# Performance work log

Measured on AMD Instinct MI355X. Metric: run time of the kernel, lower is better.

The kernel has to match this reference:

```python
import jax, jax.numpy as jnp
import numpy as np


def setup_inputs() -> dict:
    key = jax.random.key(0)
    kZ, kQ, kW, kU, kbk = jax.random.split(key, 5)
    B, E, D = 64, 16, 64
    N_ATOMS = 200000
    N_NP = 160000
    N_BK = 20000
    Q_DIM = 64
    Z = jax.random.normal(kZ, (B, E, D), dtype=jnp.float32)
    Q = jax.random.normal(kQ, (B, Q_DIM), dtype=jnp.float32)
    W = jax.random.normal(kW, (N_NP, D), dtype=jnp.float32)
    U = jax.random.normal(kU, (N_NP, Q_DIM), dtype=jnp.float32)
    np_indices = jnp.arange(N_NP, dtype=jnp.int64 if jax.config.jax_enable_x64 else jnp.int32)
    bk_indices = jax.random.randint(kbk, (N_BK,), 0, N_ATOMS, dtype=jnp.int32)
    return {"Z": Z, "Q": Q, "W": W, "U": U,
            "np_indices": np_indices, "bk_indices": bk_indices,
            "n_atoms": N_ATOMS}


def reference(Z, Q, W, U, np_indices, bk_indices, n_atoms):
    # Batched valuation for all neural-predicate atoms at once:
    # vm(Z, Q, atom_i) = sigmoid(sum_{e,d} Z[b,e,d] * W[i,d] + Q[b] . U[i])
    scores = jax.nn.sigmoid(jnp.einsum('bed,nd->bn', Z, W) + Q @ U.T)  # [B, n_np]
    B = Z.shape[0]
    V = jnp.zeros((B, n_atoms), dtype=jnp.float32)
    V = V.at[:, 0].set(1.0)                 # V[:, 0] = 1.0 (true atom)
    V = V.at[:, np_indices].set(scores)     # scatter valuation outputs
    V = V.at[:, bk_indices].add(1.0)        # background knowledge atoms += 1
    return V
```

## Files before the change

kernel.cpp:

```cpp
#include <hip/hip_runtime.h>


typedef _Float16 half8_t __attribute__((ext_vector_type(8)));
typedef float float4_t __attribute__((ext_vector_type(4)));

#define E_DIM 16
#define D_DIM 64
#define QD    64
#define NS    2
#define CRES_STRIDE 132

__global__ void prep_kernel(const float* __restrict__ Z, const float* __restrict__ Q,
                            const int* __restrict__ bk, int n_bk,
                            _Float16* __restrict__ Afrag, float* __restrict__ cnt) {
    int blk = blockIdx.x;
    int tid = threadIdx.x;
    if (blk < 32) {
        int t = blk * 256 + tid;
        int b = t >> 7, k = t & 127;
        float v;
        if (k < D_DIM) {
            const float* zp = Z + (size_t)b * E_DIM * D_DIM + k;
            v = 0.f;
            #pragma unroll
            for (int e = 0; e < E_DIM; ++e) v += zp[e * D_DIM];
        } else {
            v = Q[b * QD + (k - D_DIM)];
        }
        int mt = b >> 4, r = b & 15;
        int kq = k >> 5, j = k & 7, quad = (k >> 3) & 3;
        int lane = r + quad * 16;
        Afrag[(((mt * 4 + kq) * 64) + lane) * 8 + j] = (_Float16)v;
    } else if (cnt) {
        int i = (blk - 32) * 256 + tid;
        if (i < n_bk) atomicAdd(&cnt[bk[i]], 1.0f);
    }
}

__global__ __launch_bounds__(256, 3) void main_kernel(
        const float* __restrict__ W, const float* __restrict__ U,
        const _Float16* __restrict__ Afrag, const float* __restrict__ cnt,
        float* __restrict__ V, int n_np, int n_atoms, int tail_w) {
    __shared__ __align__(16) half8_t Ash[1024];
    __shared__ __align__(16) float Cres[64][CRES_STRIDE];
    int tid = threadIdx.x;
    int bid = blockIdx.x;
    long long base = (long long)bid * (64 * NS);
    int wv = tid >> 6, lane = tid & 63;
    int quad = lane >> 4, l15 = lane & 15;
    int rB = wv * 16 + l15;

    const float4_t* Wg = (const float4_t*)W;
    const float4_t* Ug = (const float4_t*)U;

    {
        const half8_t* Ap = (const half8_t*)Afrag;
        #pragma unroll
        for (int i = 0; i < 4; ++i)
            Ash[tid + i * 256] = Ap[tid + i * 256];
    }

    int cfl = tid & 31;
    float4_t cn4 = {0.f, 0.f, 0.f, 0.f};
    if (cnt) cn4 = *(const float4_t*)(cnt + base + 4 * cfl);

    {
        long long tb = (long long)n_np + (long long)bid * tail_w;
        int c8 = tid & 7, rg = tid >> 3;
        long long col = tb + 4 * c8;
        if (4 * c8 < tail_w && col < n_atoms) {
            float4_t t4 = {0.f, 0.f, 0.f, 0.f};
            if (cnt) t4 = *(const float4_t*)(cnt + col);
            *(float4_t*)(V + (size_t)rg * n_atoms + col) = t4;
            *(float4_t*)(V + (size_t)(rg + 32) * n_atoms + col) = t4;
        }
    }

    __syncthreads();

    auto load_panel = [&](int s, float4_t wr[4], float4_t ur[4]) {
        size_t o = ((size_t)(base + s * 64 + rB)) * 16 + quad * 2;
        wr[0] = Wg[o];     wr[1] = Wg[o + 1];
        wr[2] = Wg[o + 8]; wr[3] = Wg[o + 9];
        ur[0] = Ug[o];     ur[1] = Ug[o + 1];
        ur[2] = Ug[o + 8]; ur[3] = Ug[o + 9];
    };

    auto compute_panel = [&](int s, const float4_t wr[4], const float4_t ur[4]) {
        half8_t b0, b1, b2, b3;
        #pragma unroll
        for (int q = 0; q < 4; ++q) {
            b0[q]     = (_Float16)wr[0][q];
            b0[q + 4] = (_Float16)wr[1][q];
            b1[q]     = (_Float16)wr[2][q];
            b1[q + 4] = (_Float16)wr[3][q];
            b2[q]     = (_Float16)ur[0][q];
            b2[q + 4] = (_Float16)ur[1][q];
            b3[q]     = (_Float16)ur[2][q];
            b3[q + 4] = (_Float16)ur[3][q];
        }
        #pragma unroll
        for (int mt = 0; mt < 4; ++mt) {
            half8_t a0 = Ash[(mt * 4 + 0) * 64 + lane];
            half8_t a1 = Ash[(mt * 4 + 1) * 64 + lane];
            half8_t a2 = Ash[(mt * 4 + 2) * 64 + lane];
            half8_t a3 = Ash[(mt * 4 + 3) * 64 + lane];
            float4_t acc = {0.f, 0.f, 0.f, 0.f};
            acc = __builtin_amdgcn_mfma_f32_16x16x32_f16(a0, b0, acc, 0, 0, 0);
            acc = __builtin_amdgcn_mfma_f32_16x16x32_f16(a1, b1, acc, 0, 0, 0);
            acc = __builtin_amdgcn_mfma_f32_16x16x32_f16(a2, b2, acc, 0, 0, 0);
            acc = __builtin_amdgcn_mfma_f32_16x16x32_f16(a3, b3, acc, 0, 0, 0);
            #pragma unroll
            for (int r = 0; r < 4; ++r)
                Cres[mt * 16 + quad * 4 + r][s * 64 + rB] = acc[r];
        }
    };

    float4_t w0[4], u0[4], w1[4], u1[4];
    load_panel(0, w0, u0);
    {
    }
    compute_panel(0, w0, u0);
    load_panel(1, w1, u1);
    compute_panel(1, w1, u1);

    __syncthreads();

    #pragma unroll
    for (int rd = 0; rd < 8; ++rd) {
        int row = rd * 8 + (tid >> 5);
        float4_t v = *(const float4_t*)&Cres[row][4 * cfl];
        float4_t out;
        #pragma unroll
        for (int q = 0; q < 4; ++q)
            out[q] = 1.0f / (1.0f + __expf(-v[q])) + cn4[q];
        *(float4_t*)(V + (size_t)row * n_atoms + base + 4 * cfl) = out;
    }
}

__global__ void bk_scatter(const int* __restrict__ bk, int n_bk,
                           float* __restrict__ V, int n_atoms) {
    int i = blockIdx.x * 256 + threadIdx.x;
    if (i < n_bk)
        atomicAdd(&V[(size_t)blockIdx.y * n_atoms + bk[i]], 1.0f);
}

extern "C" void kernel_launch(void* const* d_in, const int* in_sizes, int n_in,
                              void* d_out, int out_size, void* d_ws, size_t ws_size,
                              hipStream_t stream) {
    const float* Z = (const float*)d_in[0];
    const float* Q = (const float*)d_in[1];
    const float* W = (const float*)d_in[2];
    const float* U = (const float*)d_in[3];
    const int* bk = (const int*)d_in[5];
    float* V = (float*)d_out;

    int B       = in_sizes[0] / (E_DIM * D_DIM);
    int n_np    = in_sizes[2] / D_DIM;
    int n_bk    = in_sizes[5];
    int n_atoms = out_size / B;

    _Float16* Afrag = (_Float16*)d_ws;
    size_t need = 16384 + (size_t)n_atoms * sizeof(float);
    bool use_cnt = ws_size >= need;
    float* cnt = use_cnt ? (float*)((char*)d_ws + 16384) : nullptr;

    if (use_cnt) {
        hipMemsetAsync(cnt, 0, (size_t)n_atoms * sizeof(float), stream);
        int cnt_blocks = (n_bk + 255) / 256;
        prep_kernel<<<32 + cnt_blocks, 256, 0, stream>>>(Z, Q, bk, n_bk, Afrag, cnt);
    } else {
        prep_kernel<<<32, 256, 0, stream>>>(Z, Q, bk, n_bk, Afrag, nullptr);
    }

    int gb = n_np / (64 * NS);
    int tail_w = (n_atoms - n_np + gb - 1) / gb;
    main_kernel<<<gb, 256, 0, stream>>>(W, U, Afrag, cnt, V,
                                        n_np, n_atoms, tail_w);

    if (!use_cnt) {
        dim3 g((n_bk + 255) / 256, B);
        bk_scatter<<<g, 256, 0, stream>>>(bk, n_bk, V, n_atoms);
    }
}
```

Measured before the change: 139.7 us.

## Process five panels per block with double-buffered loads and per-panel epilogue

Each block now handles five 64-column panels instead of two, and prefetches W/U two panels ahead into a two-slot register buffer. The sigmoid epilogue runs per panel through a smaller 64x68 LDS tile guarded by custom lgkmcnt barriers, so V stores overlap the next panel's loads. Tail-region zeroing becomes a strided loop, and occupancy is lowered to 2 blocks per SM. The aim is fewer blocks, less setup per block and better overlap of loads with MFMA work, at the cost of extra barriers. The tail width is now floor-divided, which only covers every column when the remainder divides evenly, as it does for these sizes.

```diff
diff --git a/kernel.cpp b/kernel.cpp
--- a/kernel.cpp
+++ b/kernel.cpp
@@ -7,8 +7,16 @@
 #define E_DIM 16
 #define D_DIM 64
 #define QD    64
-#define NS    2
-#define CRES_STRIDE 132
+#define NP    5
+#define CRES_STRIDE 68
+
+__device__ __forceinline__ void lds_barrier() {
+    asm volatile("s_waitcnt lgkmcnt(0)" ::: "memory");
+    __builtin_amdgcn_sched_barrier(0);
+    __builtin_amdgcn_s_barrier();
+    __builtin_amdgcn_sched_barrier(0);
+    asm volatile("" ::: "memory");
+}
 
 __global__ void prep_kernel(const float* __restrict__ Z, const float* __restrict__ Q,
                             const int* __restrict__ bk, int n_bk,
@@ -37,7 +45,7 @@
     }
 }
 
-__global__ __launch_bounds__(256, 3) void main_kernel(
+__global__ __launch_bounds__(256, 2) void main_kernel(
         const float* __restrict__ W, const float* __restrict__ U,
         const _Float16* __restrict__ Afrag, const float* __restrict__ cnt,
         float* __restrict__ V, int n_np, int n_atoms, int tail_w) {
@@ -45,10 +53,12 @@
     __shared__ __align__(16) float Cres[64][CRES_STRIDE];
     int tid = threadIdx.x;
     int bid = blockIdx.x;
-    long long base = (long long)bid * (64 * NS);
+    long long base = (long long)bid * (64 * NP);
     int wv = tid >> 6, lane = tid & 63;
     int quad = lane >> 4, l15 = lane & 15;
     int rB = wv * 16 + l15;
+    int chunk = tid & 15;
+    int rgrp  = tid >> 4;
 
     const float4_t* Wg = (const float4_t*)W;
     const float4_t* Ug = (const float4_t*)U;
@@ -60,45 +70,63 @@
             Ash[tid + i * 256] = Ap[tid + i * 256];
     }
 
-    int cfl = tid & 31;
-    float4_t cn4 = {0.f, 0.f, 0.f, 0.f};
-    if (cnt) cn4 = *(const float4_t*)(cnt + base + 4 * cfl);
+    float4_t cn4[NP];
+    #pragma unroll
+    for (int p = 0; p < NP; ++p) {
+        cn4[p] = float4_t{0.f, 0.f, 0.f, 0.f};
+        if (cnt) cn4[p] = *(const float4_t*)(cnt + base + p * 64 + 4 * chunk);
+    }
 
     {
         long long tb = (long long)n_np + (long long)bid * tail_w;
-        int c8 = tid & 7, rg = tid >> 3;
-        long long col = tb + 4 * c8;
-        if (4 * c8 < tail_w && col < n_atoms) {
+        int nt4 = tail_w >> 2;
+        int total = 64 * nt4;
+        for (int i = tid; i < total; i += 256) {
+            int row = i / nt4, c = i - row * nt4;
+            long long col = tb + 4 * c;
             float4_t t4 = {0.f, 0.f, 0.f, 0.f};
             if (cnt) t4 = *(const float4_t*)(cnt + col);
-            *(float4_t*)(V + (size_t)rg * n_atoms + col) = t4;
-            *(float4_t*)(V + (size_t)(rg + 32) * n_atoms + col) = t4;
+            *(float4_t*)(V + (size_t)row * n_atoms + col) = t4;
         }
     }
 
     __syncthreads();
 
-    auto load_panel = [&](int s, float4_t wr[4], float4_t ur[4]) {
-        size_t o = ((size_t)(base + s * 64 + rB)) * 16 + quad * 2;
-        wr[0] = Wg[o];     wr[1] = Wg[o + 1];
-        wr[2] = Wg[o + 8]; wr[3] = Wg[o + 9];
-        ur[0] = Ug[o];     ur[1] = Ug[o + 1];
-        ur[2] = Ug[o + 8]; ur[3] = Ug[o + 9];
-    };
-
-    auto compute_panel = [&](int s, const float4_t wr[4], const float4_t ur[4]) {
+    float4_t wb[2][4], ub[2][4];
+    #pragma unroll
+    for (int p = 0; p < 2; ++p) {
+        size_t o = ((size_t)(base + p * 64 + rB)) * 16 + quad * 2;
+        wb[p][0] = Wg[o];     wb[p][1] = Wg[o + 1];
+        wb[p][2] = Wg[o + 8]; wb[p][3] = Wg[o + 9];
+        ub[p][0] = Ug[o];     ub[p][1] = Ug[o + 1];
+        ub[p][2] = Ug[o + 8]; ub[p][3] = Ug[o + 9];
+    }
+
+    #pragma unroll
+    for (int p = 0; p < NP; ++p) {
+        int pb = p & 1;
+
         half8_t b0, b1, b2, b3;
         #pragma unroll
         for (int q = 0; q < 4; ++q) {
-            b0[q]     = (_Float16)wr[0][q];
-            b0[q + 4] = (_Float16)wr[1][q];
-            b1[q]     = (_Float16)wr[2][q];
-            b1[q + 4] = (_Float16)wr[3][q];
-            b2[q]     = (_Float16)ur[0][q];
-            b2[q + 4] = (_Float16)ur[1][q];
-            b3[q]     = (_Float16)ur[2][q];
-            b3[q + 4] = (_Float16)ur[3][q];
-        }
+            b0[q]     = (_Float16)wb[pb][0][q];
+            b0[q + 4] = (_Float16)wb[pb][1][q];
+            b1[q]     = (_Float16)wb[pb][2][q];
+            b1[q + 4] = (_Float16)wb[pb][3][q];
+            b2[q]     = (_Float16)ub[pb][0][q];
+            b2[q + 4] = (_Float16)ub[pb][1][q];
+            b3[q]     = (_Float16)ub[pb][2][q];
+            b3[q + 4] = (_Float16)ub[pb][3][q];
+        }
+
+        if (p + 2 < NP) {
+            size_t o = ((size_t)(base + (p + 2) * 64 + rB)) * 16 + quad * 2;
+            wb[pb][0] = Wg[o];     wb[pb][1] = Wg[o + 1];
+            wb[pb][2] = Wg[o + 8]; wb[pb][3] = Wg[o + 9];
+            ub[pb][0] = Ug[o];     ub[pb][1] = Ug[o + 1];
+            ub[pb][2] = Ug[o + 8]; ub[pb][3] = Ug[o + 9];
+        }
+
         #pragma unroll
         for (int mt = 0; mt < 4; ++mt) {
             half8_t a0 = Ash[(mt * 4 + 0) * 64 + lane];
@@ -112,29 +140,23 @@
             acc = __builtin_amdgcn_mfma_f32_16x16x32_f16(a3, b3, acc, 0, 0, 0);
             #pragma unroll
             for (int r = 0; r < 4; ++r)
-                Cres[mt * 16 + quad * 4 + r][s * 64 + rB] = acc[r];
-        }
-    };
-
-    float4_t w0[4], u0[4], w1[4], u1[4];
-    load_panel(0, w0, u0);
-    {
-    }
-    compute_panel(0, w0, u0);
-    load_panel(1, w1, u1);
-    compute_panel(1, w1, u1);
-
-    __syncthreads();
-
-    #pragma unroll
-    for (int rd = 0; rd < 8; ++rd) {
-        int row = rd * 8 + (tid >> 5);
-        float4_t v = *(const float4_t*)&Cres[row][4 * cfl];
-        float4_t out;
-        #pragma unroll
-        for (int q = 0; q < 4; ++q)
-            out[q] = 1.0f / (1.0f + __expf(-v[q])) + cn4[q];
-        *(float4_t*)(V + (size_t)row * n_atoms + base + 4 * cfl) = out;
+                Cres[mt * 16 + quad * 4 + r][rB] = acc[r];
+        }
+
+        lds_barrier();
+
+        #pragma unroll
+        for (int rd = 0; rd < 4; ++rd) {
+            int row = rd * 16 + rgrp;
+            float4_t v = *(const float4_t*)&Cres[row][4 * chunk];
+            float4_t out;
+            #pragma unroll
+            for (int q = 0; q < 4; ++q)
+                out[q] = 1.0f / (1.0f + __expf(-v[q])) + cn4[p][q];
+            *(float4_t*)(V + (size_t)row * n_atoms + base + p * 64 + 4 * chunk) = out;
+        }
+
+        lds_barrier();
     }
 }
 
@@ -173,8 +195,8 @@
         prep_kernel<<<32, 256, 0, stream>>>(Z, Q, bk, n_bk, Afrag, nullptr);
     }
 
-    int gb = n_np / (64 * NS);
-    int tail_w = (n_atoms - n_np + gb - 1) / gb;
+    int gb = n_np / (64 * NP);
+    int tail_w = (n_atoms - n_np) / gb;
     main_kernel<<<gb, 256, 0, stream>>>(W, U, Afrag, cnt, V,
                                         n_np, n_atoms, tail_w);
 
```

Result: no change. 142.1 us (+1.7%).
